# Kernel optimization log

Measured on AMD Instinct MI355X. Metric: run time of the kernel, lower is better.

The kernel has to match this reference:

```python
import jax, jax.numpy as jnp
import numpy as np

NQ, M, ND, N, H, DIM = 32, 32, 200, 160, 768, 128
TEMP = 0.1      # log_softmax temperature
TAU = 0.5       # gumbel-softmax temperature
NEG = -10000.0


def _l2norm(x):
    # F.normalize(p=2, dim=-1) with eps clamp
    n = jnp.maximum(jnp.linalg.norm(x, axis=-1, keepdims=True), 1e-12)
    return x / n


def setup_inputs() -> dict:
    key = jax.random.key(0)
    k1, k2, k3, k4, k5, k6 = jax.random.split(key, 6)
    Q = jax.random.normal(k1, (NQ, M, H), dtype=jnp.float32)
    D = jax.random.normal(k2, (ND, N, H), dtype=jnp.float32)
    q_mask = jax.random.randint(k3, (NQ, M), 0, 2).astype(jnp.float32)
    d_mask = jax.random.randint(k4, (ND, N), 0, 2).astype(jnp.float32)
    # pre-sampled Gumbel(0,1) noise for gumbel_softmax (fixed for determinism)
    u = jax.random.uniform(k5, (NQ, ND, M, N), dtype=jnp.float32,
                           minval=1e-6, maxval=1.0 - 1e-6)
    gumbel_noise = -jnp.log(-jnp.log(u))
    # proj_linear: Linear(768, dim, bias=False)
    W_proj = jax.random.normal(k6, (H, DIM), dtype=jnp.float32) / np.sqrt(H)
    return {"Q": Q, "D": D, "q_mask": q_mask, "d_mask": d_mask,
            "gumbel_noise": gumbel_noise, "W_proj": W_proj}


def reference(Q, D, q_mask, d_mask, gumbel_noise, W_proj):
    # project + L2-normalize token embeddings
    Qp = _l2norm(Q @ W_proj)            # [q, m, dim]
    Dp = _l2norm(D @ W_proj)            # [d, n, dim]

    # pairwise token similarities: [q, d, m, n]
    sim = jnp.einsum('qmh,dnh->qdmn', Qp, Dp)

    dm = d_mask[None, :, None, :]       # [1, d, 1, n]
    sim_masked = sim * dm + (1.0 - dm) * NEG

    logits = jax.nn.log_softmax(sim_masked / TEMP, axis=-1)

    # gumbel_softmax(tau=0.5, hard=True) with straight-through
    y_soft = jax.nn.softmax((logits + gumbel_noise) / TAU, axis=-1)
    idx = jnp.argmax(y_soft, axis=-1)
    y_hard = jax.nn.one_hot(idx, N, dtype=y_soft.dtype)
    y = jax.lax.stop_gradient(y_hard - y_soft) + y_soft

    # select doc token per query token, mask query tokens, sum -> [q, d]
    scores = (y * sim_masked).sum(-1)          # [q, d, m]
    scores = scores * q_mask[:, None, :]
    return scores.sum(-1)                      # [q, d]
```

## Files before the change

### kernel.cpp

```cpp
#include <hip/hip_runtime.h>
#include <math.h>

#define NQ_   32
#define M_    32
#define ND_   200
#define N_    160
#define H_    768
#define DIM_  128
#define DROWS_ (ND_ * N_)
#define QROWS_ (NQ_ * M_)
#define TROWS_ (DROWS_ + QROWS_)

__device__ __forceinline__ void gl_lds16(const float* g, float* l) {
    __builtin_amdgcn_global_load_lds(
        (const __attribute__((address_space(1))) unsigned int*)g,
        (__attribute__((address_space(3))) unsigned int*)l, 16, 0, 0);
}

#define ASM_VMCNT0 asm volatile("s_waitcnt vmcnt(0)" ::: "memory")
#define ASM_LGKM0  asm volatile("s_waitcnt lgkmcnt(0)" ::: "memory")

__global__ __launch_bounds__(64) void proj_kernel(
    const float* __restrict__ Dmat, const float* __restrict__ Qmat,
    const float* __restrict__ W, float* __restrict__ DpT,
    float* __restrict__ QpT)
{
    __shared__ __align__(16) float Xt[2][16][16];
    __shared__ __align__(16) float Ws[2][16][128];
    const int lane = threadIdx.x;
    const int rb   = blockIdx.x * 16;
    const int cg   = lane & 15;
    const int rg   = lane >> 4;
    const int xrow = lane >> 2;
    const int xc4  = lane & 3;

    const int rX = rb + xrow;
    const float* xr_ptr = (rX < DROWS_) ? (Dmat + (size_t)rX * H_)
                                        : (Qmat + (size_t)(rX - DROWS_) * H_);

    float acc[4][8];
#pragma unroll
    for (int i = 0; i < 4; ++i)
#pragma unroll
        for (int j = 0; j < 8; ++j) acc[i][j] = 0.0f;

#pragma unroll
    for (int t = 0; t < 8; ++t)
        gl_lds16(W + t * 256 + lane * 4, &Ws[0][0][0] + t * 256);
    float4 xreg = *reinterpret_cast<const float4*>(xr_ptr + xc4 * 4);

    for (int c = 0; c < 48; ++c) {
        const int cb = c & 1;
        Xt[cb][xc4*4+0][xrow] = xreg.x;
        Xt[cb][xc4*4+1][xrow] = xreg.y;
        Xt[cb][xc4*4+2][xrow] = xreg.z;
        Xt[cb][xc4*4+3][xrow] = xreg.w;
        ASM_VMCNT0;
        ASM_LGKM0;
        if (c < 47) {
            const int kc = (c + 1) * 16;
            const float* wsrc = W + (size_t)kc * DIM_;
            float* wdst = &Ws[cb ^ 1][0][0];
#pragma unroll
            for (int t = 0; t < 8; ++t)
                gl_lds16(wsrc + t * 256 + lane * 4, wdst + t * 256);
            xreg = *reinterpret_cast<const float4*>(xr_ptr + kc + xc4 * 4);
        }
        __builtin_amdgcn_sched_barrier(0);
#pragma unroll
        for (int k = 0; k < 16; ++k) {
            float a[4], b[8];
            *reinterpret_cast<float4*>(&a[0]) = *reinterpret_cast<const float4*>(&Xt[cb][k][rg*4]);
            *reinterpret_cast<float4*>(&b[0]) = *reinterpret_cast<const float4*>(&Ws[cb][k][cg*8]);
            *reinterpret_cast<float4*>(&b[4]) = *reinterpret_cast<const float4*>(&Ws[cb][k][cg*8+4]);
#pragma unroll
            for (int i = 0; i < 4; ++i)
#pragma unroll
                for (int j = 0; j < 8; ++j)
                    acc[i][j] = fmaf(a[i], b[j], acc[i][j]);
        }
    }

    float nrm[4];
#pragma unroll
    for (int i = 0; i < 4; ++i) {
        float ss = 0.0f;
#pragma unroll
        for (int j = 0; j < 8; ++j) ss = __fadd_rn(ss, __fmul_rn(acc[i][j], acc[i][j]));
        ss = __fadd_rn(ss, __shfl_xor(ss, 1));
        ss = __fadd_rn(ss, __shfl_xor(ss, 2));
        ss = __fadd_rn(ss, __shfl_xor(ss, 4));
        ss = __fadd_rn(ss, __shfl_xor(ss, 8));
        nrm[i] = fmaxf(sqrtf(ss), 1e-12f);
    }

    if (rb < DROWS_) {
        const int dd = rb / 160, n0 = rb - dd * 160;
        float* o = DpT + (size_t)dd * (DIM_ * N_) + n0 + rg * 4;
#pragma unroll
        for (int j = 0; j < 8; ++j) {
            float4 v;
            v.x = acc[0][j] / nrm[0];
            v.y = acc[1][j] / nrm[1];
            v.z = acc[2][j] / nrm[2];
            v.w = acc[3][j] / nrm[3];
            *reinterpret_cast<float4*>(o + (size_t)(cg*8 + j) * N_) = v;
        }
    } else {
        const int rq = rb - DROWS_;
        const int qq = rq >> 5, m0 = rq & 31;
        float* o = QpT + (size_t)qq * (DIM_ * M_) + m0 + rg * 4;
#pragma unroll
        for (int j = 0; j < 8; ++j) {
            float4 v;
            v.x = acc[0][j] / nrm[0];
            v.y = acc[1][j] / nrm[1];
            v.z = acc[2][j] / nrm[2];
            v.w = acc[3][j] / nrm[3];
            *reinterpret_cast<float4*>(o + (size_t)(cg*8 + j) * M_) = v;
        }
    }
}

__global__ __launch_bounds__(128) void score_kernel(
    const float* __restrict__ QpT, const float* __restrict__ DpT,
    const float* __restrict__ qmask, const float* __restrict__ dmask,
    const float* __restrict__ gum, float* __restrict__ out)
{
    __shared__ float Qt[2][8][32];
    __shared__ float Dt[2][8][160];
    const int tid  = threadIdx.x;
    const int lane = tid & 63;
    const int wv   = tid >> 6;
    const int mg   = lane >> 4;
    const int ng   = lane & 15;
    const int job  = blockIdx.x * 2 + wv;
    const int q    = job & 31;
    const int d    = job >> 5;

    const float* Qb = QpT + (size_t)q * (DIM_ * M_);
    const float* Db = DpT + (size_t)d * (DIM_ * N_);
    float* qt = &Qt[wv][0][0];
    float* dt = &Dt[wv][0][0];

    float acc[8][10];
#pragma unroll
    for (int i = 0; i < 8; ++i)
#pragma unroll
        for (int j = 0; j < 10; ++j) acc[i][j] = 0.0f;

    for (int kc = 0; kc < DIM_; kc += 8) {
        ASM_LGKM0;
        gl_lds16(Qb + kc * M_ + lane * 4, qt);
#pragma unroll
        for (int c = 0; c < 5; ++c)
            gl_lds16(Db + kc * N_ + c * 256 + lane * 4, dt + c * 256);
        ASM_VMCNT0;
        __builtin_amdgcn_sched_barrier(0);
#pragma unroll
        for (int k = 0; k < 8; ++k) {
            float a[8], b[10];
            *reinterpret_cast<float4*>(&a[0]) = *reinterpret_cast<const float4*>(qt + k*32 + mg*8);
            *reinterpret_cast<float4*>(&a[4]) = *reinterpret_cast<const float4*>(qt + k*32 + mg*8 + 4);
            const float* bp = dt + k*160 + ng*10;
#pragma unroll
            for (int j2 = 0; j2 < 5; ++j2)
                *reinterpret_cast<float2*>(&b[j2*2]) = *reinterpret_cast<const float2*>(&bp[j2*2]);
#pragma unroll
            for (int i = 0; i < 8; ++i)
#pragma unroll
                for (int j = 0; j < 10; ++j)
                    acc[i][j] = fmaf(a[i], b[j], acc[i][j]);
        }
    }

    float dmv[10];
#pragma unroll
    for (int j = 0; j < 10; ++j)
        dmv[j] = dmask[(size_t)d * N_ + ng*10 + j];

    const float* gq = gum + ((size_t)q * ND_ + d) * ((size_t)M_ * N_);

    float partial = 0.0f;
#pragma unroll
    for (int i = 0; i < 8; ++i) {
        const int m = mg*8 + i;
        float x[10];
        float mx = -3.402823466e38f;
#pragma unroll
        for (int j = 0; j < 10; ++j) {
            float sm = (dmv[j] != 0.0f) ? acc[i][j] : -10000.0f;
            x[j] = sm / 0.1f;
            mx = fmaxf(mx, x[j]);
        }
        mx = fmaxf(mx, __shfl_xor(mx, 1));
        mx = fmaxf(mx, __shfl_xor(mx, 2));
        mx = fmaxf(mx, __shfl_xor(mx, 4));
        mx = fmaxf(mx, __shfl_xor(mx, 8));

        float se = 0.0f;
#pragma unroll
        for (int j = 0; j < 10; ++j) se = __fadd_rn(se, expf(x[j] - mx));
        se = __fadd_rn(se, __shfl_xor(se, 1));
        se = __fadd_rn(se, __shfl_xor(se, 2));
        se = __fadd_rn(se, __shfl_xor(se, 4));
        se = __fadd_rn(se, __shfl_xor(se, 8));
        const float lse = logf(se);

        float g[10];
        const float2* gp = reinterpret_cast<const float2*>(&gq[(size_t)m * N_ + ng*10]);
#pragma unroll
        for (int j2 = 0; j2 < 5; ++j2)
            *reinterpret_cast<float2*>(&g[j2*2]) = gp[j2];

        float z[10];
        float mz = -3.402823466e38f;
#pragma unroll
        for (int j = 0; j < 10; ++j) {
            z[j] = ((x[j] - mx - lse) + g[j]) / 0.5f;
            mz = fmaxf(mz, z[j]);
        }
        mz = fmaxf(mz, __shfl_xor(mz, 1));
        mz = fmaxf(mz, __shfl_xor(mz, 2));
        mz = fmaxf(mz, __shfl_xor(mz, 4));
        mz = fmaxf(mz, __shfl_xor(mz, 8));

        float e2[10];
        float s2 = 0.0f;
#pragma unroll
        for (int j = 0; j < 10; ++j) { e2[j] = expf(z[j] - mz); s2 = __fadd_rn(s2, e2[j]); }
        s2 = __fadd_rn(s2, __shfl_xor(s2, 1));
        s2 = __fadd_rn(s2, __shfl_xor(s2, 2));
        s2 = __fadd_rn(s2, __shfl_xor(s2, 4));
        s2 = __fadd_rn(s2, __shfl_xor(s2, 8));

        float besty = -1.0f; int bestn = 0x7fffffff; float bests = 0.0f;
#pragma unroll
        for (int j = 0; j < 10; ++j) {
            float y = e2[j] / s2;
            if (y > besty) {
                besty = y;
                bestn = ng*10 + j;
                bests = (dmv[j] != 0.0f) ? acc[i][j] : -10000.0f;
            }
        }
#pragma unroll
        for (int dl = 1; dl < 16; dl <<= 1) {
            float oy = __shfl_xor(besty, dl);
            int   on = __shfl_xor(bestn, dl);
            float os = __shfl_xor(bests, dl);
            if (oy > besty || (oy == besty && on < bestn)) {
                besty = oy; bestn = on; bests = os;
            }
        }
        const float qmv = qmask[q * M_ + m];
        if (ng == 0) partial = __fadd_rn(partial, __fmul_rn(bests, qmv));
    }
    partial = __fadd_rn(partial, __shfl_xor(partial, 16));
    partial = __fadd_rn(partial, __shfl_xor(partial, 32));
    if (lane == 0) out[(size_t)q * ND_ + d] = partial;
}

extern "C" void kernel_launch(void* const* d_in, const int* in_sizes, int n_in,
                              void* d_out, int out_size, void* d_ws, size_t ws_size,
                              hipStream_t stream)
{
    const float* Q   = (const float*)d_in[0];
    const float* D   = (const float*)d_in[1];
    const float* qm  = (const float*)d_in[2];
    const float* dm  = (const float*)d_in[3];
    const float* gum = (const float*)d_in[4];
    const float* W   = (const float*)d_in[5];
    float* out = (float*)d_out;

    float* QpT = (float*)d_ws;
    float* DpT = QpT + (size_t)QROWS_ * DIM_;

    proj_kernel<<<dim3(TROWS_ / 16), dim3(64), 0, stream>>>(D, Q, W, DpT, QpT);
    score_kernel<<<dim3(NQ_ * ND_ / 2), dim3(128), 0, stream>>>(QpT, DpT, qm, dm, gum, out);
}
```

Measured before the change: 533.1 us.

## Double-buffer global-to-LDS loads in projection and score kernels with partial vmcnt waits

Both kernels now keep two chunks of loads in flight. Each waits with a partial vmcnt count, so compute on one LDS buffer overlaps the fetch of the next chunk instead of draining all loads every iteration. The score kernel also switches from two independent waves per block to one wave per block, doubling the grid, so each wave gets its own double buffer. The risks are more LDS per wave, possibly lower occupancy, and correctness that depends on the hand-counted vmcnt values.

```diff
diff --git a/kernel.cpp b/kernel.cpp
--- a/kernel.cpp
+++ b/kernel.cpp
@@ -17,8 +17,8 @@
         (__attribute__((address_space(3))) unsigned int*)l, 16, 0, 0);
 }
 
-#define ASM_VMCNT0 asm volatile("s_waitcnt vmcnt(0)" ::: "memory")
-#define ASM_LGKM0  asm volatile("s_waitcnt lgkmcnt(0)" ::: "memory")
+#define ASM_VMCNT(n) asm volatile("s_waitcnt vmcnt(" #n ")" ::: "memory")
+#define ASM_LGKM0    asm volatile("s_waitcnt lgkmcnt(0)" ::: "memory")
 
 __global__ __launch_bounds__(64) void proj_kernel(
     const float* __restrict__ Dmat, const float* __restrict__ Qmat,
@@ -47,37 +47,68 @@
 #pragma unroll
     for (int t = 0; t < 8; ++t)
         gl_lds16(W + t * 256 + lane * 4, &Ws[0][0][0] + t * 256);
-    float4 xreg = *reinterpret_cast<const float4*>(xr_ptr + xc4 * 4);
-
-    for (int c = 0; c < 48; ++c) {
-        const int cb = c & 1;
-        Xt[cb][xc4*4+0][xrow] = xreg.x;
-        Xt[cb][xc4*4+1][xrow] = xreg.y;
-        Xt[cb][xc4*4+2][xrow] = xreg.z;
-        Xt[cb][xc4*4+3][xrow] = xreg.w;
-        ASM_VMCNT0;
+    float4 xr0 = *reinterpret_cast<const float4*>(xr_ptr + xc4 * 4);
+#pragma unroll
+    for (int t = 0; t < 8; ++t)
+        gl_lds16(W + 16 * DIM_ + t * 256 + lane * 4, &Ws[1][0][0] + t * 256);
+    float4 xr1 = *reinterpret_cast<const float4*>(xr_ptr + 16 + xc4 * 4);
+
+    for (int c = 0; c < 48; c += 2) {
+        Xt[0][xc4*4+0][xrow] = xr0.x;
+        Xt[0][xc4*4+1][xrow] = xr0.y;
+        Xt[0][xc4*4+2][xrow] = xr0.z;
+        Xt[0][xc4*4+3][xrow] = xr0.w;
+        ASM_VMCNT(9);
         ASM_LGKM0;
-        if (c < 47) {
-            const int kc = (c + 1) * 16;
-            const float* wsrc = W + (size_t)kc * DIM_;
-            float* wdst = &Ws[cb ^ 1][0][0];
-#pragma unroll
-            for (int t = 0; t < 8; ++t)
-                gl_lds16(wsrc + t * 256 + lane * 4, wdst + t * 256);
-            xreg = *reinterpret_cast<const float4*>(xr_ptr + kc + xc4 * 4);
-        }
         __builtin_amdgcn_sched_barrier(0);
 #pragma unroll
         for (int k = 0; k < 16; ++k) {
             float a[4], b[8];
-            *reinterpret_cast<float4*>(&a[0]) = *reinterpret_cast<const float4*>(&Xt[cb][k][rg*4]);
-            *reinterpret_cast<float4*>(&b[0]) = *reinterpret_cast<const float4*>(&Ws[cb][k][cg*8]);
-            *reinterpret_cast<float4*>(&b[4]) = *reinterpret_cast<const float4*>(&Ws[cb][k][cg*8+4]);
+            *reinterpret_cast<float4*>(&a[0]) = *reinterpret_cast<const float4*>(&Xt[0][k][rg*4]);
+            *reinterpret_cast<float4*>(&b[0]) = *reinterpret_cast<const float4*>(&Ws[0][k][cg*8]);
+            *reinterpret_cast<float4*>(&b[4]) = *reinterpret_cast<const float4*>(&Ws[0][k][cg*8+4]);
 #pragma unroll
             for (int i = 0; i < 4; ++i)
 #pragma unroll
                 for (int j = 0; j < 8; ++j)
                     acc[i][j] = fmaf(a[i], b[j], acc[i][j]);
+        }
+        ASM_LGKM0;
+        if (c + 2 < 48) {
+            const int kc = (c + 2) * 16;
+            const float* wsrc = W + (size_t)kc * DIM_;
+#pragma unroll
+            for (int t = 0; t < 8; ++t)
+                gl_lds16(wsrc + t * 256 + lane * 4, &Ws[0][0][0] + t * 256);
+            xr0 = *reinterpret_cast<const float4*>(xr_ptr + kc + xc4 * 4);
+        }
+        Xt[1][xc4*4+0][xrow] = xr1.x;
+        Xt[1][xc4*4+1][xrow] = xr1.y;
+        Xt[1][xc4*4+2][xrow] = xr1.z;
+        Xt[1][xc4*4+3][xrow] = xr1.w;
+        ASM_VMCNT(9);
+        ASM_LGKM0;
+        __builtin_amdgcn_sched_barrier(0);
+#pragma unroll
+        for (int k = 0; k < 16; ++k) {
+            float a[4], b[8];
+            *reinterpret_cast<float4*>(&a[0]) = *reinterpret_cast<const float4*>(&Xt[1][k][rg*4]);
+            *reinterpret_cast<float4*>(&b[0]) = *reinterpret_cast<const float4*>(&Ws[1][k][cg*8]);
+            *reinterpret_cast<float4*>(&b[4]) = *reinterpret_cast<const float4*>(&Ws[1][k][cg*8+4]);
+#pragma unroll
+            for (int i = 0; i < 4; ++i)
+#pragma unroll
+                for (int j = 0; j < 8; ++j)
+                    acc[i][j] = fmaf(a[i], b[j], acc[i][j]);
+        }
+        ASM_LGKM0;
+        if (c + 3 < 48) {
+            const int kc = (c + 3) * 16;
+            const float* wsrc = W + (size_t)kc * DIM_;
+#pragma unroll
+            for (int t = 0; t < 8; ++t)
+                gl_lds16(wsrc + t * 256 + lane * 4, &Ws[1][0][0] + t * 256);
+            xr1 = *reinterpret_cast<const float4*>(xr_ptr + kc + xc4 * 4);
         }
     }
 
@@ -122,26 +153,21 @@
     }
 }
 
-__global__ __launch_bounds__(128) void score_kernel(
+__global__ __launch_bounds__(64) void score_kernel(
     const float* __restrict__ QpT, const float* __restrict__ DpT,
     const float* __restrict__ qmask, const float* __restrict__ dmask,
     const float* __restrict__ gum, float* __restrict__ out)
 {
-    __shared__ float Qt[2][8][32];
-    __shared__ float Dt[2][8][160];
-    const int tid  = threadIdx.x;
-    const int lane = tid & 63;
-    const int wv   = tid >> 6;
+    __shared__ __align__(16) float Qt[2][8][32];
+    __shared__ __align__(16) float Dt[2][8][160];
+    const int lane = threadIdx.x;
     const int mg   = lane >> 4;
     const int ng   = lane & 15;
-    const int job  = blockIdx.x * 2 + wv;
-    const int q    = job & 31;
-    const int d    = job >> 5;
+    const int q    = blockIdx.x & 31;
+    const int d    = blockIdx.x >> 5;
 
     const float* Qb = QpT + (size_t)q * (DIM_ * M_);
     const float* Db = DpT + (size_t)d * (DIM_ * N_);
-    float* qt = &Qt[wv][0][0];
-    float* dt = &Dt[wv][0][0];
 
     float acc[8][10];
 #pragma unroll
@@ -149,20 +175,37 @@
 #pragma unroll
         for (int j = 0; j < 10; ++j) acc[i][j] = 0.0f;
 
-    for (int kc = 0; kc < DIM_; kc += 8) {
-        ASM_LGKM0;
-        gl_lds16(Qb + kc * M_ + lane * 4, qt);
-#pragma unroll
-        for (int c = 0; c < 5; ++c)
-            gl_lds16(Db + kc * N_ + c * 256 + lane * 4, dt + c * 256);
-        ASM_VMCNT0;
+#define ISSUE_CHUNK(c_)                                                     \
+    do {                                                                    \
+        const int b_ = (c_) & 1;                                            \
+        const float* qs_ = Qb + (size_t)(c_) * 8 * M_;                      \
+        const float* ds_ = Db + (size_t)(c_) * 8 * N_;                      \
+        float* qd_ = &Qt[b_][0][0];                                         \
+        float* dd_ = &Dt[b_][0][0];                                         \
+        gl_lds16(qs_ + lane * 4, qd_);                                      \
+        gl_lds16(ds_ + 0    + lane * 4, dd_ + 0);                           \
+        gl_lds16(ds_ + 256  + lane * 4, dd_ + 256);                         \
+        gl_lds16(ds_ + 512  + lane * 4, dd_ + 512);                         \
+        gl_lds16(ds_ + 768  + lane * 4, dd_ + 768);                         \
+        gl_lds16(ds_ + 1024 + lane * 4, dd_ + 1024);                        \
+    } while (0)
+
+    ISSUE_CHUNK(0);
+    ISSUE_CHUNK(1);
+
+    for (int c = 0; c < 16; ++c) {
+        if (c < 15) { ASM_VMCNT(6); }
+        else        { ASM_VMCNT(0); }
         __builtin_amdgcn_sched_barrier(0);
+        const int cb = c & 1;
+        const float* qtb = &Qt[cb][0][0];
+        const float* dtb = &Dt[cb][0][0];
 #pragma unroll
         for (int k = 0; k < 8; ++k) {
             float a[8], b[10];
-            *reinterpret_cast<float4*>(&a[0]) = *reinterpret_cast<const float4*>(qt + k*32 + mg*8);
-            *reinterpret_cast<float4*>(&a[4]) = *reinterpret_cast<const float4*>(qt + k*32 + mg*8 + 4);
-            const float* bp = dt + k*160 + ng*10;
+            *reinterpret_cast<float4*>(&a[0]) = *reinterpret_cast<const float4*>(qtb + k*32 + mg*8);
+            *reinterpret_cast<float4*>(&a[4]) = *reinterpret_cast<const float4*>(qtb + k*32 + mg*8 + 4);
+            const float* bp = dtb + k*160 + ng*10;
 #pragma unroll
             for (int j2 = 0; j2 < 5; ++j2)
                 *reinterpret_cast<float2*>(&b[j2*2]) = *reinterpret_cast<const float2*>(&bp[j2*2]);
@@ -172,7 +215,12 @@
                 for (int j = 0; j < 10; ++j)
                     acc[i][j] = fmaf(a[i], b[j], acc[i][j]);
         }
-    }
+        if (c < 14) {
+            ASM_LGKM0;
+            ISSUE_CHUNK(c + 2);
+        }
+    }
+#undef ISSUE_CHUNK
 
     float dmv[10];
 #pragma unroll
@@ -277,5 +325,5 @@
     float* DpT = QpT + (size_t)QROWS_ * DIM_;
 
     proj_kernel<<<dim3(TROWS_ / 16), dim3(64), 0, stream>>>(D, Q, W, DpT, QpT);
-    score_kernel<<<dim3(NQ_ * ND_ / 2), dim3(128), 0, stream>>>(QpT, DpT, qm, dm, gum, out);
+    score_kernel<<<dim3(NQ_ * ND_), dim3(64), 0, stream>>>(QpT, DpT, qm, dm, gum, out);
 }
```

Measured after the change: 531.3 us. About the same (-0.3%).
